# Performance work log

Measured on AMD Instinct MI355X. Metric: run time of the kernel, lower is better.

## Reference

```python
import jax, jax.numpy as jnp
import numpy as np

DN = ('NCHW', 'OIHW', 'NCHW')

def conv3x3(x, w):
    return jax.lax.conv_general_dilated(x, w, (1, 1), [(1, 1), (1, 1)], dimension_numbers=DN)

def setup_inputs() -> dict:
    key = jax.random.key(0)
    ks = jax.random.split(key, 5)
    N, C, H, W = 64, 512, 16, 16
    fan = C * 3 * 3
    s = 1.0 / np.sqrt(fan)
    x = jax.random.normal(ks[0], (N, C, H, W), dtype=jnp.float32)
    Wq = jax.random.normal(ks[1], (C, C, 3, 3), dtype=jnp.float32) * s
    Wk = jax.random.normal(ks[2], (C, C, 3, 3), dtype=jnp.float32) * s
    Wv = jax.random.normal(ks[3], (C, C, 3, 3), dtype=jnp.float32) * s
    Wc = jax.random.normal(ks[4], (C, C, 3, 3), dtype=jnp.float32) * s
    gamma = jnp.ones((C,), dtype=jnp.float32)
    beta = jnp.zeros((C,), dtype=jnp.float32)
    return {"x": x, "Wq": Wq, "Wk": Wk, "Wv": Wv, "Wc": Wc, "gamma": gamma, "beta": beta}

def reference(x, Wq, Wk, Wv, Wc, gamma, beta):
    C = x.shape[1]
    q = conv3x3(x, Wq)  # [N,C,H,W]
    k = conv3x3(x, Wk)
    v = conv3x3(x, Wv)
    # att[n,m,h,w] = sum_c q[n,c,h,w] * k[m,c,h,w] / sqrt(C); softmax over m
    att = jnp.einsum('nchw,mchw->nmhw', q, k) / jnp.sqrt(jnp.float32(C))
    att = jax.nn.softmax(att, axis=1)
    # virt[n,c,h,w] = sum_m att[n,m,h,w] * v[m,c,h,w]
    virt = jnp.einsum('nmhw,mchw->nchw', att, v)
    # GroupNorm(1, C): normalize over (C,H,W) per sample, per-channel affine
    mu = jnp.mean(virt, axis=(1, 2, 3), keepdims=True)
    var = jnp.var(virt, axis=(1, 2, 3), keepdims=True)
    virt = (virt - mu) * jax.lax.rsqrt(var + 1e-5)
    virt = virt * gamma[None, :, None, None] + beta[None, :, None, None]
    virt = jax.nn.relu(virt)
    virt = conv3x3(virt, Wc)
    # Dropout is identity in eval mode
    return x + virt
```

## Files before the change

kernel.cpp:

```cpp
#include <hip/hip_runtime.h>
#include <math.h>

typedef unsigned short u16;
typedef unsigned int u32;
typedef short short8 __attribute__((ext_vector_type(8)));
typedef float f32x4 __attribute__((ext_vector_type(4)));

#define NB 64
#define CCH 512
#define HW 256

__device__ __forceinline__ u16 f2bf(float f) {
    union { float f; u32 u; } x; x.f = f;
    u32 r = x.u + 0x7fffu + ((x.u >> 16) & 1u);
    return (u16)(r >> 16);
}
__device__ __forceinline__ float bf2f(u16 b) {
    union { u32 u; float f; } x; x.u = ((u32)b) << 16;
    return x.f;
}
__device__ __forceinline__ void gload_lds16(const u16* g, u16* l) {
    __builtin_amdgcn_global_load_lds((const __attribute__((address_space(1))) u32*)g,
                                     (__attribute__((address_space(3))) u32*)l, 16, 0, 0);
}

__global__ __launch_bounds__(256) void zero_borders(u16* __restrict__ pad) {
    const int n = blockIdx.x, t = threadIdx.x;
    short8 z = (short8){0,0,0,0,0,0,0,0};
    for (int idx = t; idx < 68 * 64; idx += 256) {
        int cell = idx >> 6, ch = idx & 63;
        int hh, ww;
        if (cell < 18)      { hh = 0;          ww = cell; }
        else if (cell < 36) { hh = 17;         ww = cell - 18; }
        else if (cell < 52) { hh = cell - 35;  ww = 0; }
        else                { hh = cell - 51;  ww = 17; }
        *(short8*)(pad + ((size_t)((n * 18 + hh) * 18 + ww)) * 512 + ch * 8) = z;
    }
}

__global__ __launch_bounds__(256) void prep_x(const float* __restrict__ x, u16* __restrict__ pad) {
    __shared__ float tl[64][65];
    const int n = blockIdx.z, c0 = blockIdx.y * 64, p0 = blockIdx.x * 64;
    const int t = threadIdx.x;
    {
        const int cc = t >> 2, ps = (t & 3) * 16;
#pragma unroll
        for (int i = 0; i < 4; ++i) {
            float4 v4 = *(const float4*)(x + (((size_t)(n * 512 + c0 + cc)) << 8) + p0 + ps + i * 4);
            tl[cc][ps + i * 4 + 0] = v4.x;
            tl[cc][ps + i * 4 + 1] = v4.y;
            tl[cc][ps + i * 4 + 2] = v4.z;
            tl[cc][ps + i * 4 + 3] = v4.w;
        }
    }
    __syncthreads();
    {
        const int pp = t >> 2, cs = (t & 3) * 16;
        short8 o0, o1;
#pragma unroll
        for (int i = 0; i < 8; ++i) o0[i] = (short)f2bf(tl[cs + i][pp]);
#pragma unroll
        for (int i = 0; i < 8; ++i) o1[i] = (short)f2bf(tl[cs + 8 + i][pp]);
        const int p = p0 + pp, h = p >> 4, wcol = p & 15;
        u16* dst = pad + ((size_t)((n * 18 + h + 1) * 18 + wcol + 1)) * 512 + c0 + cs;
        *(short8*)(dst + 0) = o0;
        *(short8*)(dst + 8) = o1;
    }
}

__global__ __launch_bounds__(256) void prep_w(
    const float* __restrict__ Wq, const float* __restrict__ Wk,
    const float* __restrict__ Wv, const float* __restrict__ Wc,
    u16* __restrict__ Wt)
{
    __shared__ float lw[4608];
    const int co = blockIdx.x, sel = blockIdx.y, t = threadIdx.x;
    const float* Ws = (sel == 0) ? Wq : (sel == 1) ? Wk : (sel == 2) ? Wv : Wc;
#pragma unroll
    for (int i = 0; i < 18; ++i) lw[t + i * 256] = Ws[(size_t)co * 4608 + t + i * 256];
    __syncthreads();
    for (int tap = 0; tap < 9; ++tap)
#pragma unroll
        for (int hh = 0; hh < 2; ++hh) {
            int ci = t + hh * 256;
            Wt[(((size_t)(sel * 9 + tap)) << 18) + (co << 9) + ci] = f2bf(lw[ci * 9 + tap]);
        }
}

__global__ __launch_bounds__(512, 1) void qkv_mfma8(
    const u16* __restrict__ pad, const u16* __restrict__ Wt,
    u16* __restrict__ q, u16* __restrict__ k, u16* __restrict__ v)
{
    __shared__ short As[3][8192];
    __shared__ short Bs[3][6144];
    const int t = threadIdx.x;
    const int l = t & 63;
    const int wid = t >> 6;
    const int wm = wid >> 2, wn = wid & 3;

    const int o = blockIdx.x;
    const int wg = (o & 7) * 64 + (o >> 3);
    const int imbase = (wg >> 3) * 256;
    const int cobase = (wg & 7) * 192;

    const int cl = ((l & 3) - ((l >> 3) & 3)) & 3;
    int imoffA[2], woffB[2];
#pragma unroll
    for (int rr = 0; rr < 2; ++rr) {
        const int chunk = wid * 2 + rr;
        const int imrow = imbase + chunk * 16 + (l >> 2);
        const int p = imrow >> 6, n = imrow & 63;
        imoffA[rr] = ((n * 18 + (p >> 4)) * 18 + (p & 15)) * 512 + cl * 8;
        const int cof = cobase + chunk * 16 + (l >> 2);
        const int sel = cof >> 9, co = cof & 511;
        woffB[rr] = sel * 9 * 262144 + co * 512 + cl * 8;
    }

    const int fp = ((l >> 4) + (l >> 1)) & 3;
    const int aoff = (wm * 128 + (l & 15)) * 32 + fp * 8;
    const int boff = (wn * 48 + (l & 15)) * 32 + fp * 8;

    f32x4 acc[8][3];
#pragma unroll
    for (int i = 0; i < 8; ++i)
#pragma unroll
        for (int j = 0; j < 3; ++j) acc[i][j] = (f32x4){0.f, 0.f, 0.f, 0.f};

    auto STAGE_A = [&](int kt, int s) {
        const int tap = kt >> 4;
        const int shift = ((tap / 3) * 18 + (tap % 3)) * 512 + (kt & 15) * 32;
#pragma unroll
        for (int rr = 0; rr < 2; ++rr)
            gload_lds16(pad + imoffA[rr] + shift, (u16*)(&As[s][0] + (wid * 2 + rr) * 512));
    };
    auto STAGE_B = [&](int kt, int s) {
        if (wid < 6) {
            const int tap = kt >> 4;
            const int shift = tap * 262144 + (kt & 15) * 32;
#pragma unroll
            for (int rr = 0; rr < 2; ++rr)
                gload_lds16(Wt + woffB[rr] + shift, (u16*)(&Bs[s][0] + (wid * 2 + rr) * 512));
        }
    };

    STAGE_A(0, 0); STAGE_B(0, 0);
    STAGE_A(1, 1); STAGE_B(1, 1);
    if (wid < 6) asm volatile("s_waitcnt vmcnt(4)" ::: "memory");
    else         asm volatile("s_waitcnt vmcnt(2)" ::: "memory");
    __builtin_amdgcn_sched_barrier(0);
    __builtin_amdgcn_s_barrier();
    __builtin_amdgcn_sched_barrier(0);

    int s0 = 0;
    short8 fa[4], fa2[4], fb[3];
#pragma unroll 1
    for (int kt = 0; kt < 144; ++kt) {
        const int s2 = (s0 == 0) ? 2 : s0 - 1;
        const short* Ab = &As[s0][0];
        const short* Bb = &Bs[s0][0];

#pragma unroll
        for (int j = 0; j < 3; ++j) fb[j] = *(const short8*)(Bb + boff + j * 512);
#pragma unroll
        for (int i = 0; i < 4; ++i) fa[i] = *(const short8*)(Ab + aoff + i * 512);
        if (kt < 142) STAGE_A(kt + 2, s2);
        __builtin_amdgcn_sched_barrier(0);
        __builtin_amdgcn_s_barrier();
        asm volatile("s_waitcnt lgkmcnt(0)" ::: "memory");
        __builtin_amdgcn_sched_barrier(0);
        __builtin_amdgcn_s_setprio(1);
#pragma unroll
        for (int i = 0; i < 4; ++i)
#pragma unroll
            for (int j = 0; j < 3; ++j)
                acc[i][j] = __builtin_amdgcn_mfma_f32_16x16x32_bf16(fa[i], fb[j], acc[i][j], 0, 0, 0);
        __builtin_amdgcn_s_setprio(0);
        __builtin_amdgcn_sched_barrier(0);
        __builtin_amdgcn_s_barrier();

#pragma unroll
        for (int i = 0; i < 4; ++i) fa2[i] = *(const short8*)(Ab + aoff + 2048 + i * 512);
        if (kt < 142) STAGE_B(kt + 2, s2);
        __builtin_amdgcn_sched_barrier(0);
        __builtin_amdgcn_s_barrier();
        asm volatile("s_waitcnt lgkmcnt(0)" ::: "memory");
        __builtin_amdgcn_sched_barrier(0);
        __builtin_amdgcn_s_setprio(1);
#pragma unroll
        for (int i = 0; i < 4; ++i)
#pragma unroll
            for (int j = 0; j < 3; ++j)
                acc[4 + i][j] = __builtin_amdgcn_mfma_f32_16x16x32_bf16(fa2[i], fb[j], acc[4 + i][j], 0, 0, 0);
        __builtin_amdgcn_s_setprio(0);
        if (kt >= 142) {
            asm volatile("s_waitcnt vmcnt(0)" ::: "memory");
        } else if (wid < 6) {
            asm volatile("s_waitcnt vmcnt(4)" ::: "memory");
        } else {
            asm volatile("s_waitcnt vmcnt(2)" ::: "memory");
        }
        __builtin_amdgcn_sched_barrier(0);
        __builtin_amdgcn_s_barrier();
        __builtin_amdgcn_sched_barrier(0);

        s0 = (s0 == 2) ? 0 : s0 + 1;
    }

#pragma unroll
    for (int j = 0; j < 3; ++j) {
        const int colb = cobase + wn * 48 + j * 16;
        u16* op = ((colb >> 9) == 0) ? q : (((colb >> 9) == 1) ? k : v);
        op += (colb & 511) + (l & 15);
#pragma unroll
        for (int i = 0; i < 8; ++i) {
            const int row = imbase + wm * 128 + i * 16 + (l >> 4) * 4;
#pragma unroll
            for (int r = 0; r < 4; ++r)
                op[(size_t)(row + r) * 512] = f2bf(acc[i][j][r]);
        }
    }
}

__global__ __launch_bounds__(512, 1) void cres_pipe(
    const u16* __restrict__ pad, const u16* __restrict__ WtC,
    const float* __restrict__ xres, float* __restrict__ out)
{
    __shared__ short As[4][4096];
    __shared__ short Bs[4][8192];
    const int t = threadIdx.x;
    const int l = t & 63;
    const int wid = t >> 6;
    const int wm = wid >> 2, wn = wid & 3;

    const int cobase = (blockIdx.x & 3) * 128;
    const int imbase = (blockIdx.x >> 2) * 256;

    const int cl = ((l & 3) - ((l >> 3) & 3)) & 3;
    int woffA, imoffB[2];
    {
        const int co = cobase + wid * 16 + (l >> 2);
        woffA = co * 512 + cl * 8;
    }
#pragma unroll
    for (int rr = 0; rr < 2; ++rr) {
        const int u = wid * 2 + rr;
        const int imrow = imbase + u * 16 + (l >> 2);
        const int n = imrow >> 8, p = imrow & 255;
        imoffB[rr] = ((n * 18 + (p >> 4)) * 18 + (p & 15)) * 512 + cl * 8;
    }

    const int fp = ((l >> 4) + (l >> 1)) & 3;
    const int aoff = (wm * 64 + (l & 15)) * 32 + fp * 8;
    const int boff = (wn * 64 + (l & 15)) * 32 + fp * 8;

    f32x4 acc[4][4];
#pragma unroll
    for (int i = 0; i < 4; ++i)
#pragma unroll
        for (int j = 0; j < 4; ++j) acc[i][j] = (f32x4){0.f, 0.f, 0.f, 0.f};

    auto STAGE_CA = [&](int kt, int s) {
        const int tap = kt >> 4;
        const int shift = tap * 262144 + (kt & 15) * 32;
        gload_lds16(WtC + woffA + shift, (u16*)(&As[s][0] + wid * 512));
    };
    auto STAGE_CB = [&](int kt, int s) {
        const int tap = kt >> 4;
        const int shift = ((tap / 3) * 18 + (tap % 3)) * 512 + (kt & 15) * 32;
#pragma unroll
        for (int rr = 0; rr < 2; ++rr)
            gload_lds16(pad + imoffB[rr] + shift, (u16*)(&Bs[s][0] + (wid * 2 + rr) * 512));
    };

    STAGE_CA(0, 0); STAGE_CB(0, 0);
    STAGE_CA(1, 1); STAGE_CB(1, 1);
    STAGE_CA(2, 2); STAGE_CB(2, 2);
    asm volatile("s_waitcnt vmcnt(6)" ::: "memory");
    __builtin_amdgcn_sched_barrier(0);
    __builtin_amdgcn_s_barrier();
    __builtin_amdgcn_sched_barrier(0);

    short8 A0[4], A1[4], B0[4], B1[4];
#pragma unroll
    for (int i = 0; i < 4; ++i) A0[i] = *(const short8*)(&As[0][0] + aoff + i * 512);
#pragma unroll
    for (int j = 0; j < 4; ++j) B0[j] = *(const short8*)(&Bs[0][0] + boff + j * 512);

#define CSTEP(KT, BUFR, BUFS, AM, BMF, AR, BRF)                                   \
    {                                                                             \
        if ((KT) >= 142) asm volatile("s_waitcnt vmcnt(0)" ::: "memory");         \
        else             asm volatile("s_waitcnt vmcnt(3)" ::: "memory");         \
        __builtin_amdgcn_sched_barrier(0);                                        \
        __builtin_amdgcn_s_barrier();                                             \
        __builtin_amdgcn_sched_barrier(0);                                        \
        if ((KT) < 143) {                                                         \
            const short* Abr = &As[BUFR][0];                                      \
            const short* Bbr = &Bs[BUFR][0];                                      \
            _Pragma("unroll")                                                     \
            for (int i = 0; i < 4; ++i) AR[i] = *(const short8*)(Abr + aoff + i * 512);  \
            _Pragma("unroll")                                                     \
            for (int j = 0; j < 4; ++j) BRF[j] = *(const short8*)(Bbr + boff + j * 512); \
        }                                                                         \
        if ((KT) + 3 < 144) { STAGE_CA((KT) + 3, BUFS); STAGE_CB((KT) + 3, BUFS); } \
        __builtin_amdgcn_s_setprio(1);                                            \
        _Pragma("unroll")                                                         \
        for (int i = 0; i < 4; ++i)                                               \
            _Pragma("unroll")                                                     \
            for (int j = 0; j < 4; ++j)                                           \
                acc[i][j] = __builtin_amdgcn_mfma_f32_16x16x32_bf16(AM[i], BMF[j], acc[i][j], 0, 0, 0); \
        __builtin_amdgcn_s_setprio(0);                                            \
    }

#pragma unroll 1
    for (int kt = 0; kt < 144; kt += 4) {
        CSTEP(kt + 0, 1, 3, A0, B0, A1, B1);
        CSTEP(kt + 1, 2, 0, A1, B1, A0, B0);
        CSTEP(kt + 2, 3, 1, A0, B0, A1, B1);
        CSTEP(kt + 3, 0, 2, A1, B1, A0, B0);
    }
#undef CSTEP

#pragma unroll
    for (int i = 0; i < 4; ++i)
#pragma unroll
        for (int j = 0; j < 4; ++j)
#pragma unroll
            for (int r = 0; r < 4; ++r) {
                int co = cobase + wm * 64 + i * 16 + (l >> 4) * 4 + r;
                int imrow = imbase + wn * 64 + j * 16 + (l & 15);
                int n = imrow >> 8, p = imrow & 255;
                size_t addr = (((size_t)(n * 512 + co)) << 8) + p;
                out[addr] = acc[i][j][r] + xres[addr];
            }
}

__global__ __launch_bounds__(256) void attn_kernel(
    const u16* __restrict__ qT, const u16* __restrict__ kT, u16* vvT)
{
    const int p = blockIdx.x;
    const int t = threadIdx.x;
    __shared__ float smemA[2][64][68];
    __shared__ float attb[64][68];
    const size_t pb = (size_t)p * (NB * CCH);

    const int ng = t >> 4, mg = t & 15;
    const int n0 = ng * 4, m0 = mg * 4;
    float acc[4][4];
#pragma unroll
    for (int i = 0; i < 4; ++i)
#pragma unroll
        for (int j = 0; j < 4; ++j) acc[i][j] = 0.f;

    for (int ct = 0; ct < 8; ++ct) {
        const int c0 = ct * 64;
        __syncthreads();
#pragma unroll
        for (int s = 0; s < 2; ++s) {
            int f = t + s * 256;
            int nn = f >> 3, c8 = (f & 7) * 8;
            short8 qv = *(const short8*)(qT + pb + (size_t)nn * CCH + c0 + c8);
            short8 kv = *(const short8*)(kT + pb + (size_t)nn * CCH + c0 + c8);
#pragma unroll
            for (int e = 0; e < 8; ++e) {
                smemA[0][nn][c8 + e] = bf2f((u16)qv[e]);
                smemA[1][nn][c8 + e] = bf2f((u16)kv[e]);
            }
        }
        __syncthreads();
#pragma unroll 4
        for (int c4 = 0; c4 < 16; ++c4) {
            float4 q4[4], k4[4];
#pragma unroll
            for (int i = 0; i < 4; ++i) q4[i] = *(const float4*)&smemA[0][n0 + i][c4 * 4];
#pragma unroll
            for (int j = 0; j < 4; ++j) k4[j] = *(const float4*)&smemA[1][m0 + j][c4 * 4];
#pragma unroll
            for (int i = 0; i < 4; ++i)
#pragma unroll
                for (int j = 0; j < 4; ++j) {
                    acc[i][j] = fmaf(q4[i].x, k4[j].x, acc[i][j]);
                    acc[i][j] = fmaf(q4[i].y, k4[j].y, acc[i][j]);
                    acc[i][j] = fmaf(q4[i].z, k4[j].z, acc[i][j]);
                    acc[i][j] = fmaf(q4[i].w, k4[j].w, acc[i][j]);
                }
        }
    }

    const float SCALE = 0.0441941738241592f;
#pragma unroll
    for (int i = 0; i < 4; ++i) {
        float m = fmaxf(fmaxf(acc[i][0], acc[i][1]), fmaxf(acc[i][2], acc[i][3]));
#pragma unroll
        for (int mask = 1; mask < 16; mask <<= 1) m = fmaxf(m, __shfl_xor(m, mask, 16));
        float e[4]; float s = 0.f;
#pragma unroll
        for (int j = 0; j < 4; ++j) { e[j] = __expf((acc[i][j] - m) * SCALE); s += e[j]; }
#pragma unroll
        for (int mask = 1; mask < 16; mask <<= 1) s += __shfl_xor(s, mask, 16);
        float inv = 1.f / s;
#pragma unroll
        for (int j = 0; j < 4; ++j) attb[n0 + i][m0 + j] = e[j] * inv;
    }
    __syncthreads();

    float* vs = &smemA[0][0][0];
    const int ng2 = t >> 3, cg = t & 7;
    const int nn0 = ng2 * 2, cb = cg * 16;
    for (int ct4 = 0; ct4 < 4; ++ct4) {
        const int c0 = ct4 * 128;
#pragma unroll
        for (int s = 0; s < 4; ++s) {
            int f = t + s * 256;
            int m = f >> 4, c8 = (f & 15) * 8;
            short8 vv = *(const short8*)(vvT + pb + (size_t)m * CCH + c0 + c8);
#pragma unroll
            for (int e = 0; e < 8; ++e) vs[m * 132 + c8 + e] = bf2f((u16)vv[e]);
        }
        __syncthreads();
        float acc2[2][16];
#pragma unroll
        for (int i = 0; i < 2; ++i)
#pragma unroll
            for (int j = 0; j < 16; ++j) acc2[i][j] = 0.f;
#pragma unroll 4
        for (int m = 0; m < 64; ++m) {
            float a0 = attb[nn0][m], a1 = attb[nn0 + 1][m];
#pragma unroll
            for (int k4 = 0; k4 < 4; ++k4) {
                float4 v4 = *(const float4*)&vs[m * 132 + cb + k4 * 4];
                acc2[0][k4 * 4 + 0] = fmaf(a0, v4.x, acc2[0][k4 * 4 + 0]);
                acc2[0][k4 * 4 + 1] = fmaf(a0, v4.y, acc2[0][k4 * 4 + 1]);
                acc2[0][k4 * 4 + 2] = fmaf(a0, v4.z, acc2[0][k4 * 4 + 2]);
                acc2[0][k4 * 4 + 3] = fmaf(a0, v4.w, acc2[0][k4 * 4 + 3]);
                acc2[1][k4 * 4 + 0] = fmaf(a1, v4.x, acc2[1][k4 * 4 + 0]);
                acc2[1][k4 * 4 + 1] = fmaf(a1, v4.y, acc2[1][k4 * 4 + 1]);
                acc2[1][k4 * 4 + 2] = fmaf(a1, v4.z, acc2[1][k4 * 4 + 2]);
                acc2[1][k4 * 4 + 3] = fmaf(a1, v4.w, acc2[1][k4 * 4 + 3]);
            }
        }
#pragma unroll
        for (int i = 0; i < 2; ++i)
#pragma unroll
            for (int j = 0; j < 16; ++j)
                vvT[pb + (size_t)(nn0 + i) * CCH + c0 + cb + j] = f2bf(acc2[i][j]);
        __syncthreads();
    }
}

__global__ __launch_bounds__(256) void gn_part1(
    const u16* __restrict__ virtT, float* __restrict__ partials)
{
    const int n = blockIdx.x >> 2, qr = blockIdx.x & 3, t = threadIdx.x;
    float sum = 0.f, ss = 0.f;
#pragma unroll 4
    for (int it = 0; it < 16; ++it) {
        int f = t + it * 256;
        int p = qr * 64 + (f >> 6), c = (f & 63) * 8;
        short8 vv = *(const short8*)(virtT + ((size_t)(p * 64 + n)) * 512 + c);
#pragma unroll
        for (int e = 0; e < 8; ++e) { float x = bf2f((u16)vv[e]); sum += x; ss = fmaf(x, x, ss); }
    }
#pragma unroll
    for (int off = 32; off > 0; off >>= 1) {
        sum += __shfl_down(sum, off);
        ss  += __shfl_down(ss, off);
    }
    __shared__ float rs[4], rss[4];
    const int wid = t >> 6, lane = t & 63;
    if (lane == 0) { rs[wid] = sum; rss[wid] = ss; }
    __syncthreads();
    if (t == 0) {
        partials[(n * 4 + qr) * 2 + 0] = rs[0] + rs[1] + rs[2] + rs[3];
        partials[(n * 4 + qr) * 2 + 1] = rss[0] + rss[1] + rss[2] + rss[3];
    }
}

__global__ __launch_bounds__(256) void gn_part2(
    const u16* __restrict__ virtT, const float* __restrict__ partials,
    const float* __restrict__ gamma, const float* __restrict__ beta,
    u16* __restrict__ ypad)
{
    const int n = blockIdx.x >> 2, qr = blockIdx.x & 3, t = threadIdx.x;
    __shared__ float sg[512], sb[512];
    for (int i = t; i < 512; i += 256) { sg[i] = gamma[i]; sb[i] = beta[i]; }
    float S = 0.f, SS = 0.f;
#pragma unroll
    for (int i = 0; i < 4; ++i) {
        S  += partials[(n * 4 + i) * 2 + 0];
        SS += partials[(n * 4 + i) * 2 + 1];
    }
    const float mu = S * (1.f / 131072.f);
    const float var = SS * (1.f / 131072.f) - mu * mu;
    const float rstd = rsqrtf(var + 1e-5f);
    __syncthreads();

#pragma unroll 4
    for (int it = 0; it < 16; ++it) {
        int f = t + it * 256;
        int p = qr * 64 + (f >> 6), cc = (f & 63) * 8;
        short8 vv = *(const short8*)(virtT + ((size_t)(p * 64 + n)) * 512 + cc);
        short8 ov;
#pragma unroll
        for (int e = 0; e < 8; ++e) {
            float x = (bf2f((u16)vv[e]) - mu) * rstd;
            x = fmaf(x, sg[cc + e], sb[cc + e]);
            ov[e] = (short)f2bf(fmaxf(x, 0.f));
        }
        int h = p >> 4, wcol = p & 15;
        *(short8*)(ypad + ((size_t)((n * 18 + h + 1) * 18 + wcol + 1)) * 512 + cc) = ov;
    }
}

extern "C" void kernel_launch(void* const* d_in, const int* in_sizes, int n_in,
                              void* d_out, int out_size, void* d_ws, size_t ws_size,
                              hipStream_t stream)
{
    const float* x     = (const float*)d_in[0];
    const float* Wq    = (const float*)d_in[1];
    const float* Wk    = (const float*)d_in[2];
    const float* Wv    = (const float*)d_in[3];
    const float* Wc    = (const float*)d_in[4];
    const float* gamma = (const float*)d_in[5];
    const float* beta  = (const float*)d_in[6];
    float* out = (float*)d_out;

    u16* pad = (u16*)d_ws;
    u16* Wt  = pad + 10616832;
    u16* q   = Wt + 9437184;
    u16* k   = q + 8388608;
    u16* v   = k + 8388608;
    float* gnp = (float*)k;

    zero_borders<<<dim3(64), dim3(256), 0, stream>>>(pad);
    prep_x<<<dim3(4, 8, 64), dim3(256), 0, stream>>>(x, pad);
    prep_w<<<dim3(512, 4), dim3(256), 0, stream>>>(Wq, Wk, Wv, Wc, Wt);

    qkv_mfma8<<<dim3(512), dim3(512), 0, stream>>>(pad, Wt, q, k, v);
    attn_kernel<<<dim3(256), dim3(256), 0, stream>>>(q, k, v);
    gn_part1<<<dim3(256), dim3(256), 0, stream>>>(v, gnp);
    gn_part2<<<dim3(256), dim3(256), 0, stream>>>(v, gnp, gamma, beta, pad);
    cres_pipe<<<dim3(256), dim3(512), 0, stream>>>(pad, Wt + 3 * 2359296, x, out);
}
```

Baseline: 420.9 us.

## Shrink QKV and output conv GEMM tiles to 4-wave blocks with two blocks per CU

Both implicit-GEMM conv kernels move from 512-thread blocks (one per CU) to 256-thread blocks with launch bounds allowing two per CU. The QKV kernel's M tile is halved to 128 rows, and the output conv's tile drops from 256x128 to 128x128, which doubles the grid sizes. The pipeline is simplified to a single barrier per k-step with three LDS buffers. The intent is to overlap work across co-resident blocks instead of relying on intra-block split phases. In exchange, the grid-block swizzle is dropped and each block re-reads more shared operands, and the per-step schedule is less finely interleaved.

```diff
diff --git a/kernel.cpp b/kernel.cpp
--- a/kernel.cpp
+++ b/kernel.cpp
@@ -87,38 +87,39 @@
         }
 }
 
-__global__ __launch_bounds__(512, 1) void qkv_mfma8(
+__global__ __launch_bounds__(256, 2) void qkv_mfma4(
     const u16* __restrict__ pad, const u16* __restrict__ Wt,
     u16* __restrict__ q, u16* __restrict__ k, u16* __restrict__ v)
 {
-    __shared__ short As[3][8192];
+    __shared__ short As[3][4096];
     __shared__ short Bs[3][6144];
     const int t = threadIdx.x;
     const int l = t & 63;
     const int wid = t >> 6;
-    const int wm = wid >> 2, wn = wid & 3;
 
     const int o = blockIdx.x;
-    const int wg = (o & 7) * 64 + (o >> 3);
-    const int imbase = (wg >> 3) * 256;
-    const int cobase = (wg & 7) * 192;
+    const int imbase = (o >> 3) * 128;
+    const int cobase = (o & 7) * 192;
 
     const int cl = ((l & 3) - ((l >> 3) & 3)) & 3;
-    int imoffA[2], woffB[2];
+    int imoffA[2], woffB[3];
 #pragma unroll
     for (int rr = 0; rr < 2; ++rr) {
         const int chunk = wid * 2 + rr;
         const int imrow = imbase + chunk * 16 + (l >> 2);
         const int p = imrow >> 6, n = imrow & 63;
         imoffA[rr] = ((n * 18 + (p >> 4)) * 18 + (p & 15)) * 512 + cl * 8;
-        const int cof = cobase + chunk * 16 + (l >> 2);
+    }
+#pragma unroll
+    for (int rr = 0; rr < 3; ++rr) {
+        const int cof = cobase + (wid * 3 + rr) * 16 + (l >> 2);
         const int sel = cof >> 9, co = cof & 511;
         woffB[rr] = sel * 9 * 262144 + co * 512 + cl * 8;
     }
 
     const int fp = ((l >> 4) + (l >> 1)) & 3;
-    const int aoff = (wm * 128 + (l & 15)) * 32 + fp * 8;
-    const int boff = (wn * 48 + (l & 15)) * 32 + fp * 8;
+    const int aoff = (l & 15) * 32 + fp * 8;
+    const int boff = (wid * 48 + (l & 15)) * 32 + fp * 8;
 
     f32x4 acc[8][3];
 #pragma unroll
@@ -126,199 +127,149 @@
 #pragma unroll
         for (int j = 0; j < 3; ++j) acc[i][j] = (f32x4){0.f, 0.f, 0.f, 0.f};
 
-    auto STAGE_A = [&](int kt, int s) {
+    auto STAGE = [&](int kt, int s) {
         const int tap = kt >> 4;
-        const int shift = ((tap / 3) * 18 + (tap % 3)) * 512 + (kt & 15) * 32;
+        const int ashift = ((tap / 3) * 18 + (tap % 3)) * 512 + (kt & 15) * 32;
+        const int bshift = tap * 262144 + (kt & 15) * 32;
 #pragma unroll
         for (int rr = 0; rr < 2; ++rr)
-            gload_lds16(pad + imoffA[rr] + shift, (u16*)(&As[s][0] + (wid * 2 + rr) * 512));
+            gload_lds16(pad + imoffA[rr] + ashift, (u16*)(&As[s][0] + (wid * 2 + rr) * 512));
+#pragma unroll
+        for (int rr = 0; rr < 3; ++rr)
+            gload_lds16(Wt + woffB[rr] + bshift, (u16*)(&Bs[s][0] + (wid * 3 + rr) * 512));
     };
-    auto STAGE_B = [&](int kt, int s) {
-        if (wid < 6) {
-            const int tap = kt >> 4;
-            const int shift = tap * 262144 + (kt & 15) * 32;
-#pragma unroll
-            for (int rr = 0; rr < 2; ++rr)
-                gload_lds16(Wt + woffB[rr] + shift, (u16*)(&Bs[s][0] + (wid * 2 + rr) * 512));
-        }
-    };
-
-    STAGE_A(0, 0); STAGE_B(0, 0);
-    STAGE_A(1, 1); STAGE_B(1, 1);
-    if (wid < 6) asm volatile("s_waitcnt vmcnt(4)" ::: "memory");
-    else         asm volatile("s_waitcnt vmcnt(2)" ::: "memory");
-    __builtin_amdgcn_sched_barrier(0);
-    __builtin_amdgcn_s_barrier();
-    __builtin_amdgcn_sched_barrier(0);
+
+    STAGE(0, 0);
+    STAGE(1, 1);
 
     int s0 = 0;
-    short8 fa[4], fa2[4], fb[3];
+    short8 fa[8], fb[3];
 #pragma unroll 1
     for (int kt = 0; kt < 144; ++kt) {
         const int s2 = (s0 == 0) ? 2 : s0 - 1;
         const short* Ab = &As[s0][0];
         const short* Bb = &Bs[s0][0];
 
-#pragma unroll
-        for (int j = 0; j < 3; ++j) fb[j] = *(const short8*)(Bb + boff + j * 512);
-#pragma unroll
-        for (int i = 0; i < 4; ++i) fa[i] = *(const short8*)(Ab + aoff + i * 512);
-        if (kt < 142) STAGE_A(kt + 2, s2);
+        if (kt >= 143) asm volatile("s_waitcnt vmcnt(0)" ::: "memory");
+        else           asm volatile("s_waitcnt vmcnt(5)" ::: "memory");
         __builtin_amdgcn_sched_barrier(0);
         __builtin_amdgcn_s_barrier();
-        asm volatile("s_waitcnt lgkmcnt(0)" ::: "memory");
         __builtin_amdgcn_sched_barrier(0);
+
+#pragma unroll
+        for (int j = 0; j < 3; ++j) fb[j] = *(const short8*)(Bb + boff + j * 512);
+#pragma unroll
+        for (int i = 0; i < 8; ++i) fa[i] = *(const short8*)(Ab + aoff + i * 512);
+
+        if (kt < 142) STAGE(kt + 2, s2);
+
         __builtin_amdgcn_s_setprio(1);
 #pragma unroll
-        for (int i = 0; i < 4; ++i)
+        for (int i = 0; i < 8; ++i)
 #pragma unroll
             for (int j = 0; j < 3; ++j)
                 acc[i][j] = __builtin_amdgcn_mfma_f32_16x16x32_bf16(fa[i], fb[j], acc[i][j], 0, 0, 0);
         __builtin_amdgcn_s_setprio(0);
-        __builtin_amdgcn_sched_barrier(0);
-        __builtin_amdgcn_s_barrier();
-
-#pragma unroll
-        for (int i = 0; i < 4; ++i) fa2[i] = *(const short8*)(Ab + aoff + 2048 + i * 512);
-        if (kt < 142) STAGE_B(kt + 2, s2);
-        __builtin_amdgcn_sched_barrier(0);
-        __builtin_amdgcn_s_barrier();
-        asm volatile("s_waitcnt lgkmcnt(0)" ::: "memory");
-        __builtin_amdgcn_sched_barrier(0);
-        __builtin_amdgcn_s_setprio(1);
-#pragma unroll
-        for (int i = 0; i < 4; ++i)
-#pragma unroll
-            for (int j = 0; j < 3; ++j)
-                acc[4 + i][j] = __builtin_amdgcn_mfma_f32_16x16x32_bf16(fa2[i], fb[j], acc[4 + i][j], 0, 0, 0);
-        __builtin_amdgcn_s_setprio(0);
-        if (kt >= 142) {
-            asm volatile("s_waitcnt vmcnt(0)" ::: "memory");
-        } else if (wid < 6) {
-            asm volatile("s_waitcnt vmcnt(4)" ::: "memory");
-        } else {
-            asm volatile("s_waitcnt vmcnt(2)" ::: "memory");
-        }
+
+        s0 = (s0 == 2) ? 0 : s0 + 1;
+    }
+
+#pragma unroll
+    for (int j = 0; j < 3; ++j) {
+        const int colb = cobase + wid * 48 + j * 16;
+        u16* op = ((colb >> 9) == 0) ? q : (((colb >> 9) == 1) ? k : v);
+        op += (colb & 511) + (l & 15);
+#pragma unroll
+        for (int i = 0; i < 8; ++i) {
+            const int row = imbase + i * 16 + (l >> 4) * 4;
+#pragma unroll
+            for (int r = 0; r < 4; ++r)
+                op[(size_t)(row + r) * 512] = f2bf(acc[i][j][r]);
+        }
+    }
+}
+
+__global__ __launch_bounds__(256, 2) void cres_mfma4(
+    const u16* __restrict__ pad, const u16* __restrict__ WtC,
+    const float* __restrict__ xres, float* __restrict__ out)
+{
+    __shared__ short As[3][4096];
+    __shared__ short Bs[3][4096];
+    const int t = threadIdx.x;
+    const int l = t & 63;
+    const int wid = t >> 6;
+    const int wm = wid >> 1, wn = wid & 1;
+
+    const int o = blockIdx.x;
+    const int cobase = (o & 3) * 128;
+    const int imbase = (o >> 2) * 128;
+
+    const int cl = ((l & 3) - ((l >> 3) & 3)) & 3;
+    int woffA[2], imoffB[2];
+#pragma unroll
+    for (int rr = 0; rr < 2; ++rr) {
+        const int co = cobase + (wid * 2 + rr) * 16 + (l >> 2);
+        woffA[rr] = co * 512 + cl * 8;
+        const int imrow = imbase + (wid * 2 + rr) * 16 + (l >> 2);
+        const int n = imrow >> 8, p = imrow & 255;
+        imoffB[rr] = ((n * 18 + (p >> 4)) * 18 + (p & 15)) * 512 + cl * 8;
+    }
+
+    const int fp = ((l >> 4) + (l >> 1)) & 3;
+    const int aoff = (wm * 64 + (l & 15)) * 32 + fp * 8;
+    const int boff = (wn * 64 + (l & 15)) * 32 + fp * 8;
+
+    f32x4 acc[4][4];
+#pragma unroll
+    for (int i = 0; i < 4; ++i)
+#pragma unroll
+        for (int j = 0; j < 4; ++j) acc[i][j] = (f32x4){0.f, 0.f, 0.f, 0.f};
+
+    auto STAGE = [&](int kt, int s) {
+        const int tap = kt >> 4;
+        const int ashift = tap * 262144 + (kt & 15) * 32;
+        const int bshift = ((tap / 3) * 18 + (tap % 3)) * 512 + (kt & 15) * 32;
+#pragma unroll
+        for (int rr = 0; rr < 2; ++rr) {
+            gload_lds16(WtC + woffA[rr] + ashift, (u16*)(&As[s][0] + (wid * 2 + rr) * 512));
+            gload_lds16(pad + imoffB[rr] + bshift, (u16*)(&Bs[s][0] + (wid * 2 + rr) * 512));
+        }
+    };
+
+    STAGE(0, 0);
+    STAGE(1, 1);
+
+    int s0 = 0;
+    short8 fa[4], fb[4];
+#pragma unroll 1
+    for (int kt = 0; kt < 144; ++kt) {
+        const int s2 = (s0 == 0) ? 2 : s0 - 1;
+        const short* Ab = &As[s0][0];
+        const short* Bb = &Bs[s0][0];
+
+        if (kt >= 143) asm volatile("s_waitcnt vmcnt(0)" ::: "memory");
+        else           asm volatile("s_waitcnt vmcnt(4)" ::: "memory");
         __builtin_amdgcn_sched_barrier(0);
         __builtin_amdgcn_s_barrier();
         __builtin_amdgcn_sched_barrier(0);
 
+#pragma unroll
+        for (int i = 0; i < 4; ++i) fa[i] = *(const short8*)(Ab + aoff + i * 512);
+#pragma unroll
+        for (int j = 0; j < 4; ++j) fb[j] = *(const short8*)(Bb + boff + j * 512);
+
+        if (kt < 142) STAGE(kt + 2, s2);
+
+        __builtin_amdgcn_s_setprio(1);
+#pragma unroll
+        for (int i = 0; i < 4; ++i)
+#pragma unroll
+            for (int j = 0; j < 4; ++j)
+                acc[i][j] = __builtin_amdgcn_mfma_f32_16x16x32_bf16(fa[i], fb[j], acc[i][j], 0, 0, 0);
+        __builtin_amdgcn_s_setprio(0);
+
         s0 = (s0 == 2) ? 0 : s0 + 1;
     }
-
-#pragma unroll
-    for (int j = 0; j < 3; ++j) {
-        const int colb = cobase + wn * 48 + j * 16;
-        u16* op = ((colb >> 9) == 0) ? q : (((colb >> 9) == 1) ? k : v);
-        op += (colb & 511) + (l & 15);
-#pragma unroll
-        for (int i = 0; i < 8; ++i) {
-            const int row = imbase + wm * 128 + i * 16 + (l >> 4) * 4;
-#pragma unroll
-            for (int r = 0; r < 4; ++r)
-                op[(size_t)(row + r) * 512] = f2bf(acc[i][j][r]);
-        }
-    }
-}
-
-__global__ __launch_bounds__(512, 1) void cres_pipe(
-    const u16* __restrict__ pad, const u16* __restrict__ WtC,
-    const float* __restrict__ xres, float* __restrict__ out)
-{
-    __shared__ short As[4][4096];
-    __shared__ short Bs[4][8192];
-    const int t = threadIdx.x;
-    const int l = t & 63;
-    const int wid = t >> 6;
-    const int wm = wid >> 2, wn = wid & 3;
-
-    const int cobase = (blockIdx.x & 3) * 128;
-    const int imbase = (blockIdx.x >> 2) * 256;
-
-    const int cl = ((l & 3) - ((l >> 3) & 3)) & 3;
-    int woffA, imoffB[2];
-    {
-        const int co = cobase + wid * 16 + (l >> 2);
-        woffA = co * 512 + cl * 8;
-    }
-#pragma unroll
-    for (int rr = 0; rr < 2; ++rr) {
-        const int u = wid * 2 + rr;
-        const int imrow = imbase + u * 16 + (l >> 2);
-        const int n = imrow >> 8, p = imrow & 255;
-        imoffB[rr] = ((n * 18 + (p >> 4)) * 18 + (p & 15)) * 512 + cl * 8;
-    }
-
-    const int fp = ((l >> 4) + (l >> 1)) & 3;
-    const int aoff = (wm * 64 + (l & 15)) * 32 + fp * 8;
-    const int boff = (wn * 64 + (l & 15)) * 32 + fp * 8;
-
-    f32x4 acc[4][4];
-#pragma unroll
-    for (int i = 0; i < 4; ++i)
-#pragma unroll
-        for (int j = 0; j < 4; ++j) acc[i][j] = (f32x4){0.f, 0.f, 0.f, 0.f};
-
-    auto STAGE_CA = [&](int kt, int s) {
-        const int tap = kt >> 4;
-        const int shift = tap * 262144 + (kt & 15) * 32;
-        gload_lds16(WtC + woffA + shift, (u16*)(&As[s][0] + wid * 512));
-    };
-    auto STAGE_CB = [&](int kt, int s) {
-        const int tap = kt >> 4;
-        const int shift = ((tap / 3) * 18 + (tap % 3)) * 512 + (kt & 15) * 32;
-#pragma unroll
-        for (int rr = 0; rr < 2; ++rr)
-            gload_lds16(pad + imoffB[rr] + shift, (u16*)(&Bs[s][0] + (wid * 2 + rr) * 512));
-    };
-
-    STAGE_CA(0, 0); STAGE_CB(0, 0);
-    STAGE_CA(1, 1); STAGE_CB(1, 1);
-    STAGE_CA(2, 2); STAGE_CB(2, 2);
-    asm volatile("s_waitcnt vmcnt(6)" ::: "memory");
-    __builtin_amdgcn_sched_barrier(0);
-    __builtin_amdgcn_s_barrier();
-    __builtin_amdgcn_sched_barrier(0);
-
-    short8 A0[4], A1[4], B0[4], B1[4];
-#pragma unroll
-    for (int i = 0; i < 4; ++i) A0[i] = *(const short8*)(&As[0][0] + aoff + i * 512);
-#pragma unroll
-    for (int j = 0; j < 4; ++j) B0[j] = *(const short8*)(&Bs[0][0] + boff + j * 512);
-
-#define CSTEP(KT, BUFR, BUFS, AM, BMF, AR, BRF)                                   \
-    {                                                                             \
-        if ((KT) >= 142) asm volatile("s_waitcnt vmcnt(0)" ::: "memory");         \
-        else             asm volatile("s_waitcnt vmcnt(3)" ::: "memory");         \
-        __builtin_amdgcn_sched_barrier(0);                                        \
-        __builtin_amdgcn_s_barrier();                                             \
-        __builtin_amdgcn_sched_barrier(0);                                        \
-        if ((KT) < 143) {                                                         \
-            const short* Abr = &As[BUFR][0];                                      \
-            const short* Bbr = &Bs[BUFR][0];                                      \
-            _Pragma("unroll")                                                     \
-            for (int i = 0; i < 4; ++i) AR[i] = *(const short8*)(Abr + aoff + i * 512);  \
-            _Pragma("unroll")                                                     \
-            for (int j = 0; j < 4; ++j) BRF[j] = *(const short8*)(Bbr + boff + j * 512); \
-        }                                                                         \
-        if ((KT) + 3 < 144) { STAGE_CA((KT) + 3, BUFS); STAGE_CB((KT) + 3, BUFS); } \
-        __builtin_amdgcn_s_setprio(1);                                            \
-        _Pragma("unroll")                                                         \
-        for (int i = 0; i < 4; ++i)                                               \
-            _Pragma("unroll")                                                     \
-            for (int j = 0; j < 4; ++j)                                           \
-                acc[i][j] = __builtin_amdgcn_mfma_f32_16x16x32_bf16(AM[i], BMF[j], acc[i][j], 0, 0, 0); \
-        __builtin_amdgcn_s_setprio(0);                                            \
-    }
-
-#pragma unroll 1
-    for (int kt = 0; kt < 144; kt += 4) {
-        CSTEP(kt + 0, 1, 3, A0, B0, A1, B1);
-        CSTEP(kt + 1, 2, 0, A1, B1, A0, B0);
-        CSTEP(kt + 2, 3, 1, A0, B0, A1, B1);
-        CSTEP(kt + 3, 0, 2, A1, B1, A0, B0);
-    }
-#undef CSTEP
 
 #pragma unroll
     for (int i = 0; i < 4; ++i)
@@ -535,9 +486,9 @@
     prep_x<<<dim3(4, 8, 64), dim3(256), 0, stream>>>(x, pad);
     prep_w<<<dim3(512, 4), dim3(256), 0, stream>>>(Wq, Wk, Wv, Wc, Wt);
 
-    qkv_mfma8<<<dim3(512), dim3(512), 0, stream>>>(pad, Wt, q, k, v);
+    qkv_mfma4<<<dim3(1024), dim3(256), 0, stream>>>(pad, Wt, q, k, v);
     attn_kernel<<<dim3(256), dim3(256), 0, stream>>>(q, k, v);
     gn_part1<<<dim3(256), dim3(256), 0, stream>>>(v, gnp);
     gn_part2<<<dim3(256), dim3(256), 0, stream>>>(v, gnp, gamma, beta, pad);
-    cres_pipe<<<dim3(256), dim3(512), 0, stream>>>(pad, Wt + 3 * 2359296, x, out);
-}
+    cres_mfma4<<<dim3(512), dim3(256), 0, stream>>>(pad, Wt + 3 * 2359296, x, out);
+}
```

New measurement: 436.6 us. 3.7% more time.
